# Kernel tuning notes

Hardware: AMD Instinct MI355X
Metric: run time of the kernel (lower is better)

Reference implementation:

```python
import jax, jax.numpy as jnp
import numpy as np

N = 50000      # nodes
E = 800000     # edges
INS = 128
H = 128
OUTS = 128
G = 512        # graphs in batch
BN_EPS = 1e-5


def _lin(k, fan_in, fan_out):
    s = 1.0 / np.sqrt(fan_in)
    kw, kb = jax.random.split(k)
    w = jax.random.uniform(kw, (fan_in, fan_out), minval=-s, maxval=s, dtype=jnp.float32)
    b = jax.random.uniform(kb, (fan_out,), minval=-s, maxval=s, dtype=jnp.float32)
    return w, b


def setup_inputs() -> dict:
    key = jax.random.key(0)
    ks = jax.random.split(key, 16)
    x = jax.random.normal(ks[0], (N, INS), dtype=jnp.float32)
    edge_src = jax.random.randint(ks[1], (E,), 0, N, dtype=jnp.int32)
    edge_dst = jax.random.randint(ks[2], (E,), 0, N, dtype=jnp.int32)
    ptr = jnp.sort(jax.random.randint(ks[3], (G + 1,), 0, N, dtype=jnp.int32))
    ptr = ptr.at[0].set(0).at[-1].set(N)
    w1a, b1a = _lin(ks[4], INS, H)
    w1b, b1b = _lin(ks[5], H, H)
    w2a, b2a = _lin(ks[6], H, H)
    w2b, b2b = _lin(ks[7], H, H)
    w3a, b3a = _lin(ks[8], H, H)
    w3b, b3b = _lin(ks[9], H, OUTS)
    g1 = jnp.ones((H,), jnp.float32); be1 = jnp.zeros((H,), jnp.float32)
    g2 = jnp.ones((H,), jnp.float32); be2 = jnp.zeros((H,), jnp.float32)
    g3 = jnp.ones((H,), jnp.float32); be3 = jnp.zeros((H,), jnp.float32)
    return dict(x=x, edge_src=edge_src, edge_dst=edge_dst, ptr=ptr,
                w1a=w1a, b1a=b1a, g1=g1, be1=be1, w1b=w1b, b1b=b1b,
                w2a=w2a, b2a=b2a, g2=g2, be2=be2, w2b=w2b, b2b=b2b,
                w3a=w3a, b3a=b3a, g3=g3, be3=be3, w3b=w3b, b3b=b3b)


def _bn(h, gamma, beta):
    # BatchNorm1d in training mode: stats over the node dimension
    mu = jnp.mean(h, axis=0)
    var = jnp.var(h, axis=0)
    return gamma * (h - mu) * jax.lax.rsqrt(var + BN_EPS) + beta


def _gin_layer(h, src, dst, wa, ba, gamma, beta, wb, bb):
    # GINConv (eps=0): mlp(x + sum_{j in N(i)} x_j)
    agg = jax.ops.segment_sum(h[src], dst, num_segments=N)  # [N, d]
    h = h + agg
    h = jax.nn.relu(_bn(h @ wa + ba, gamma, beta))
    h = jax.nn.relu(h @ wb + bb)
    return h


def reference(x, edge_src, edge_dst, ptr,
              w1a, b1a, g1, be1, w1b, b1b,
              w2a, b2a, g2, be2, w2b, b2b,
              w3a, b3a, g3, be3, w3b, b3b):
    h = _gin_layer(x, edge_src, edge_dst, w1a, b1a, g1, be1, w1b, b1b)
    h = _gin_layer(h, edge_src, edge_dst, w2a, b2a, g2, be2, w2b, b2b)
    h = _gin_layer(h, edge_src, edge_dst, w3a, b3a, g3, be3, w3b, b3b)
    # segment_csr(x, ptr, reduce='sum') readout
    seg = jnp.searchsorted(ptr, jnp.arange(N, dtype=jnp.int32), side='right') - 1
    return jax.ops.segment_sum(h, seg, num_segments=G)  # [G, OUTS]
```

## Files before the change

### kernel.cpp

```cpp
#include <hip/hip_runtime.h>

#define NNODES 50000
#define NEDGES 800000
#define HD 128
#define NG 512
#define BN_EPS 1e-5f
#define NTILE 3125
#define NSPLIT 8
#define NSB 49
#define AROW 136

typedef short bf16x8 __attribute__((ext_vector_type(8)));
typedef float floatx4 __attribute__((ext_vector_type(4)));

union U16 { uint4 u; bf16x8 h; };

__device__ __forceinline__ ushort f2bf(float f) {
    unsigned u = __float_as_uint(f);
    return (ushort)((u + 0x7fffu + ((u >> 16) & 1u)) >> 16);
}
__device__ __forceinline__ void unpack8(const uint4& u, float* f) {
    const unsigned* w = (const unsigned*)&u;
#pragma unroll
    for (int i = 0; i < 4; ++i) {
        f[2 * i]     = __uint_as_float(w[i] << 16);
        f[2 * i + 1] = __uint_as_float(w[i] & 0xffff0000u);
    }
}
__device__ __forceinline__ uint4 pack8(const float* f) {
    uint4 o;
    unsigned* w = (unsigned*)&o;
#pragma unroll
    for (int i = 0; i < 4; ++i)
        w[i] = (unsigned)f2bf(f[2 * i]) | ((unsigned)f2bf(f[2 * i + 1]) << 16);
    return o;
}


struct WP6 { const float* w[6]; };

__global__ __launch_bounds__(256) void prep_kernel(
    const int* __restrict__ edst, int* __restrict__ cnt, int* __restrict__ rank,
    WP6 p, ushort* __restrict__ wf) {
    const int b = blockIdx.x, t = threadIdx.x;
    if (b < 3125) {
        int i = b * 256 + t;
        rank[i] = atomicAdd(&cnt[edst[i]], 1);
    } else {
        int m = b - 3125;
        const float* W = p.w[m];
        ushort* o = wf + (size_t)m * 16384;
        for (int i = t; i < 16384; i += 256) {
            int j = i & 7, lane = (i >> 3) & 63, kc = (i >> 9) & 3, ct = i >> 11;
            int k = kc * 32 + (lane >> 4) * 8 + j;
            int n = ct * 16 + (lane & 15);
            o[i] = f2bf(W[k * HD + n]);
        }
    }
}


__global__ void scan1_kernel(const int* __restrict__ cnt, int* __restrict__ incl,
                             int* __restrict__ bsum, int n) {
    __shared__ int s[1024];
    int i = blockIdx.x * 1024 + threadIdx.x;
    int v = (i < n) ? cnt[i] : 0;
    s[threadIdx.x] = v;
    __syncthreads();
    for (int off = 1; off < 1024; off <<= 1) {
        int add = (threadIdx.x >= off) ? s[threadIdx.x - off] : 0;
        __syncthreads();
        s[threadIdx.x] += add;
        __syncthreads();
    }
    if (i < n) incl[i] = s[threadIdx.x];
    if (threadIdx.x == 1023) bsum[blockIdx.x] = s[1023];
}

__global__ void scan23_kernel(const int* __restrict__ incl, const int* __restrict__ bsum,
                              int* __restrict__ rowp, int n) {
    __shared__ int bpre[64];
    const int t = threadIdx.x;
    if (t < 64) {
        int own = (t < NSB) ? bsum[t] : 0;
        int v = own;
        for (int off = 1; off < 64; off <<= 1) {
            int u = __shfl_up(v, off);
            if (t >= off) v += u;
        }
        bpre[t] = v - own;
    }
    __syncthreads();
    int i = blockIdx.x * 256 + t;
    if (i < n) rowp[i + 1] = incl[i] + bpre[i >> 10];
    if (i == 0) rowp[0] = 0;
}

__global__ void build_kernel(const int* __restrict__ src, const int* __restrict__ dst,
                             const int* __restrict__ rowp, const int* __restrict__ rank,
                             int* __restrict__ colv, int n) {
    int i = blockIdx.x * 256 + threadIdx.x;
    if (i < n) colv[rowp[dst[i]] + rank[i]] = src[i];
}


__global__ __launch_bounds__(256, 4) void gemm0A_kernel(
    const float* __restrict__ x, const ushort* __restrict__ Wf,
    ushort* __restrict__ y) {
    __shared__ ushort abuf[16 * AROW];
    __shared__ ushort cbuf[16 * HD];
    const int t = threadIdx.x;
    const int wave = t >> 6, lane = t & 63;
    const int quad = lane >> 4, l16 = lane & 15;
    const int row0 = blockIdx.x * 16;

    const uint4* Wf4 = (const uint4*)Wf;
    uint4 bfr[2][4];
#pragma unroll
    for (int c = 0; c < 2; ++c)
#pragma unroll
        for (int kc = 0; kc < 4; ++kc)
            bfr[c][kc] = Wf4[((2 * wave + c) * 4 + kc) * 64 + lane];

    {
        int r = t >> 4, l = t & 15;
        const float* xp = x + (size_t)(row0 + r) * HD + l * 8;
        float4 v0 = ((const float4*)xp)[0];
        float4 v1 = ((const float4*)xp)[1];
        float f[8] = {v0.x, v0.y, v0.z, v0.w, v1.x, v1.y, v1.z, v1.w};
        *(uint4*)&abuf[r * AROW + l * 8] = pack8(f);
    }
    __syncthreads();

    U16 afr[4];
#pragma unroll
    for (int kc = 0; kc < 4; ++kc)
        afr[kc].u = *(const uint4*)&abuf[l16 * AROW + kc * 32 + quad * 8];

    floatx4 zf = {0.f, 0.f, 0.f, 0.f};
    floatx4 acc[2] = {zf, zf};
#pragma unroll
    for (int kc = 0; kc < 4; ++kc)
#pragma unroll
        for (int c = 0; c < 2; ++c) {
            U16 bu; bu.u = bfr[c][kc];
            acc[c] = __builtin_amdgcn_mfma_f32_16x16x32_bf16(afr[kc].h, bu.h, acc[c], 0, 0, 0);
        }

    const int lrow = quad * 4;
#pragma unroll
    for (int c = 0; c < 2; ++c) {
        int col = (2 * wave + c) * 16 + l16;
#pragma unroll
        for (int reg = 0; reg < 4; ++reg)
            cbuf[(lrow + reg) * HD + col] = f2bf(acc[c][reg]);
    }
    __syncthreads();
    {
        const uint4* c4 = (const uint4*)cbuf;
        uint4* o4 = (uint4*)y;
        int row = t >> 4, part = t & 15;
        o4[(size_t)(row0 + row) * 16 + part] = c4[t];
    }
}


__global__ __launch_bounds__(256) void agg_kernel(
    const ushort* __restrict__ y, const int* __restrict__ rowp,
    const int* __restrict__ colv, const float* __restrict__ bias,
    ushort* __restrict__ z, float* __restrict__ ssum_p, float* __restrict__ ssq_p) {
    __shared__ float reds[4][HD];
    __shared__ float redq[4][HD];
    const int t = threadIdx.x;
    const int wave = t >> 6, lane = t & 63;
    const int node = blockIdx.x * 16 + (t >> 4);
    const int l = t & 15;
    const uint4* hp = (const uint4*)y;

    float a[8];
    unpack8(hp[(size_t)node * 16 + l], a);
    int beg = rowp[node], end = rowp[node + 1];
    for (int j = beg; j < end; ++j) {
        float b[8];
        unpack8(hp[(size_t)colv[j] * 16 + l], b);
#pragma unroll
        for (int i = 0; i < 8; ++i) a[i] += b[i];
    }
    {
        float4 b0 = ((const float4*)(bias + l * 8))[0];
        float4 b1 = ((const float4*)(bias + l * 8))[1];
        a[0] += b0.x; a[1] += b0.y; a[2] += b0.z; a[3] += b0.w;
        a[4] += b1.x; a[5] += b1.y; a[6] += b1.z; a[7] += b1.w;
    }
    ((uint4*)z)[(size_t)node * 16 + l] = pack8(a);

    float s[8], q[8];
#pragma unroll
    for (int i = 0; i < 8; ++i) { s[i] = a[i]; q[i] = a[i] * a[i]; }
#pragma unroll
    for (int i = 0; i < 8; ++i) {
        s[i] += __shfl_xor(s[i], 16); s[i] += __shfl_xor(s[i], 32);
        q[i] += __shfl_xor(q[i], 16); q[i] += __shfl_xor(q[i], 32);
    }
    if (lane < 16) {
#pragma unroll
        for (int i = 0; i < 8; ++i) {
            reds[wave][lane * 8 + i] = s[i];
            redq[wave][lane * 8 + i] = q[i];
        }
    }
    __syncthreads();
    int slot = (blockIdx.x & (NSPLIT - 1)) * HD;
    if (t < HD) {
        atomicAdd(&ssum_p[slot + t], reds[0][t] + reds[1][t] + reds[2][t] + reds[3][t]);
    } else if (t < 2 * HD) {
        int c = t - HD;
        atomicAdd(&ssq_p[slot + c], redq[0][c] + redq[1][c] + redq[2][c] + redq[3][c]);
    }
}


__global__ __launch_bounds__(256, 3) void gemmBA_kernel(
    const ushort* __restrict__ z, const ushort* __restrict__ WfB,
    const ushort* __restrict__ WfA2, const float* __restrict__ biasB,
    ushort* __restrict__ yout,
    const float* __restrict__ gamma, const float* __restrict__ beta,
    const float* __restrict__ ssum_p, const float* __restrict__ ssq_p) {
    __shared__ ushort was[16384];
    __shared__ ushort cbuf[16 * AROW];
    __shared__ float sca[HD];
    __shared__ float shf[HD];
    const int t = threadIdx.x;
    const int wave = t >> 6, lane = t & 63;
    const int quad = lane >> 4, l16 = lane & 15;
    const int row0 = blockIdx.x * 16;
    const int rowA = row0 + l16;

    {
        const uint4* g = (const uint4*)WfA2;
        uint4 v[8];
#pragma unroll
        for (int i = 0; i < 8; ++i) v[i] = g[i * 256 + t];
        uint4* s = (uint4*)was;
#pragma unroll
        for (int i = 0; i < 8; ++i) s[i * 256 + t] = v[i];
    }

    const uint4* Wf4 = (const uint4*)WfB;
    uint4 bfr[2][4];
#pragma unroll
    for (int c = 0; c < 2; ++c)
#pragma unroll
        for (int kc = 0; kc < 4; ++kc)
            bfr[c][kc] = Wf4[((2 * wave + c) * 4 + kc) * 64 + lane];

    U16 afr[4];
    {
        const ushort* ap = z + (size_t)rowA * HD + quad * 8;
#pragma unroll
        for (int kc = 0; kc < 4; ++kc)
            afr[kc].u = *(const uint4*)(ap + kc * 32);
    }

    if (t < HD) {
        float s = 0.f, q = 0.f;
#pragma unroll
        for (int i = 0; i < NSPLIT; ++i) { s += ssum_p[i * HD + t]; q += ssq_p[i * HD + t]; }
        float mean = s / (float)NNODES;
        float var = q / (float)NNODES - mean * mean;
        float rstd = rsqrtf(var + BN_EPS);
        float sc = gamma[t] * rstd;
        sca[t] = sc;
        shf[t] = beta[t] - mean * sc;
    }
    __syncthreads();

#pragma unroll
    for (int kc = 0; kc < 4; ++kc) {
        float f[8];
        unpack8(afr[kc].u, f);
        int kb = kc * 32 + quad * 8;
        float4 s0 = ((const float4*)(sca + kb))[0];
        float4 s1 = ((const float4*)(sca + kb))[1];
        float4 h0 = ((const float4*)(shf + kb))[0];
        float4 h1 = ((const float4*)(shf + kb))[1];
        f[0] = fmaxf(fmaf(f[0], s0.x, h0.x), 0.f);
        f[1] = fmaxf(fmaf(f[1], s0.y, h0.y), 0.f);
        f[2] = fmaxf(fmaf(f[2], s0.z, h0.z), 0.f);
        f[3] = fmaxf(fmaf(f[3], s0.w, h0.w), 0.f);
        f[4] = fmaxf(fmaf(f[4], s1.x, h1.x), 0.f);
        f[5] = fmaxf(fmaf(f[5], s1.y, h1.y), 0.f);
        f[6] = fmaxf(fmaf(f[6], s1.z, h1.z), 0.f);
        f[7] = fmaxf(fmaf(f[7], s1.w, h1.w), 0.f);
        afr[kc].u = pack8(f);
    }

    floatx4 zf = {0.f, 0.f, 0.f, 0.f};
    floatx4 acc[2] = {zf, zf};
#pragma unroll
    for (int kc = 0; kc < 4; ++kc)
#pragma unroll
        for (int c = 0; c < 2; ++c) {
            U16 bu; bu.u = bfr[c][kc];
            acc[c] = __builtin_amdgcn_mfma_f32_16x16x32_bf16(afr[kc].h, bu.h, acc[c], 0, 0, 0);
        }

    const int lrow = quad * 4;
#pragma unroll
    for (int c = 0; c < 2; ++c) {
        int col = (2 * wave + c) * 16 + l16;
        float b = biasB[col];
#pragma unroll
        for (int reg = 0; reg < 4; ++reg)
            cbuf[(lrow + reg) * AROW + col] = f2bf(fmaxf(acc[c][reg] + b, 0.f));
    }
    __syncthreads();

    U16 a2[4];
#pragma unroll
    for (int kc = 0; kc < 4; ++kc)
        a2[kc].u = *(const uint4*)&cbuf[l16 * AROW + kc * 32 + quad * 8];
    const uint4* W2 = (const uint4*)was;
    floatx4 acc2[2] = {zf, zf};
#pragma unroll
    for (int kc = 0; kc < 4; ++kc)
#pragma unroll
        for (int c = 0; c < 2; ++c) {
            U16 bu; bu.u = W2[((2 * wave + c) * 4 + kc) * 64 + lane];
            acc2[c] = __builtin_amdgcn_mfma_f32_16x16x32_bf16(a2[kc].h, bu.h, acc2[c], 0, 0, 0);
        }
    __syncthreads();

#pragma unroll
    for (int c = 0; c < 2; ++c) {
        int col = (2 * wave + c) * 16 + l16;
#pragma unroll
        for (int reg = 0; reg < 4; ++reg)
            cbuf[(lrow + reg) * AROW + col] = f2bf(acc2[c][reg]);
    }
    __syncthreads();
    {
        uint4* o4 = (uint4*)yout;
        int row = t >> 4, part = t & 15;
        o4[(size_t)(row0 + row) * 16 + part] = *(const uint4*)&cbuf[row * AROW + part * 8];
    }
}


__global__ __launch_bounds__(256, 4) void gemmB2_kernel(
    const ushort* __restrict__ z, const ushort* __restrict__ WfB,
    const float* __restrict__ biasB,
    const float* __restrict__ gamma, const float* __restrict__ beta,
    const float* __restrict__ ssum_p, const float* __restrict__ ssq_p,
    const int* __restrict__ gptr, float* __restrict__ gout) {
    __shared__ float sca[HD];
    __shared__ float shf[HD];
    const int t = threadIdx.x;
    const int wave = t >> 6, lane = t & 63;
    const int quad = lane >> 4, l16 = lane & 15;
    const int row0 = blockIdx.x * 16;
    const int rowA = row0 + l16;

    const uint4* Wf4 = (const uint4*)WfB;
    uint4 bfr[2][4];
#pragma unroll
    for (int c = 0; c < 2; ++c)
#pragma unroll
        for (int kc = 0; kc < 4; ++kc)
            bfr[c][kc] = Wf4[((2 * wave + c) * 4 + kc) * 64 + lane];

    U16 afr[4];
    {
        const ushort* ap = z + (size_t)rowA * HD + quad * 8;
#pragma unroll
        for (int kc = 0; kc < 4; ++kc)
            afr[kc].u = *(const uint4*)(ap + kc * 32);
    }

    if (t < HD) {
        float s = 0.f, q = 0.f;
#pragma unroll
        for (int i = 0; i < NSPLIT; ++i) { s += ssum_p[i * HD + t]; q += ssq_p[i * HD + t]; }
        float mean = s / (float)NNODES;
        float var = q / (float)NNODES - mean * mean;
        float rstd = rsqrtf(var + BN_EPS);
        float sc = gamma[t] * rstd;
        sca[t] = sc;
        shf[t] = beta[t] - mean * sc;
    }
    __syncthreads();

#pragma unroll
    for (int kc = 0; kc < 4; ++kc) {
        float f[8];
        unpack8(afr[kc].u, f);
        int kb = kc * 32 + quad * 8;
        float4 s0 = ((const float4*)(sca + kb))[0];
        float4 s1 = ((const float4*)(sca + kb))[1];
        float4 h0 = ((const float4*)(shf + kb))[0];
        float4 h1 = ((const float4*)(shf + kb))[1];
        f[0] = fmaxf(fmaf(f[0], s0.x, h0.x), 0.f);
        f[1] = fmaxf(fmaf(f[1], s0.y, h0.y), 0.f);
        f[2] = fmaxf(fmaf(f[2], s0.z, h0.z), 0.f);
        f[3] = fmaxf(fmaf(f[3], s0.w, h0.w), 0.f);
        f[4] = fmaxf(fmaf(f[4], s1.x, h1.x), 0.f);
        f[5] = fmaxf(fmaf(f[5], s1.y, h1.y), 0.f);
        f[6] = fmaxf(fmaf(f[6], s1.z, h1.z), 0.f);
        f[7] = fmaxf(fmaf(f[7], s1.w, h1.w), 0.f);
        afr[kc].u = pack8(f);
    }

    floatx4 zf = {0.f, 0.f, 0.f, 0.f};
    floatx4 acc[2] = {zf, zf};
#pragma unroll
    for (int kc = 0; kc < 4; ++kc)
#pragma unroll
        for (int c = 0; c < 2; ++c) {
            U16 bu; bu.u = bfr[c][kc];
            acc[c] = __builtin_amdgcn_mfma_f32_16x16x32_bf16(afr[kc].h, bu.h, acc[c], 0, 0, 0);
        }

    int r_base = row0 + quad * 4;
    int lo = 0, hi = NG - 1;
    while (lo < hi) {
        int mid = (lo + hi) >> 1;
        if (r_base >= gptr[mid + 1]) lo = mid + 1; else hi = mid;
    }
    int segr[4];
    int sg = lo;
#pragma unroll
    for (int reg = 0; reg < 4; ++reg) {
        while (r_base + reg >= gptr[sg + 1]) ++sg;
        segr[reg] = sg;
    }
#pragma unroll
    for (int c = 0; c < 2; ++c) {
        int col = (2 * wave + c) * 16 + l16;
        float b = biasB[col];
        float run = 0.f;
        int cur = segr[0];
#pragma unroll
        for (int reg = 0; reg < 4; ++reg) {
            if (segr[reg] != cur) {
                if (run != 0.f) atomicAdd(&gout[cur * HD + col], run);
                run = 0.f;
                cur = segr[reg];
            }
            run += fmaxf(acc[c][reg] + b, 0.f);
        }
        if (run != 0.f) atomicAdd(&gout[cur * HD + col], run);
    }
}


extern "C" void kernel_launch(void* const* d_in, const int* in_sizes, int n_in,
                              void* d_out, int out_size, void* d_ws, size_t ws_size,
                              hipStream_t stream) {
    const float* x = (const float*)d_in[0];
    const int* esrc = (const int*)d_in[1];
    const int* edst = (const int*)d_in[2];
    const int* gptr = (const int*)d_in[3];
    const float* wA[3] = {(const float*)d_in[4], (const float*)d_in[10], (const float*)d_in[16]};
    const float* bA[3] = {(const float*)d_in[5], (const float*)d_in[11], (const float*)d_in[17]};
    const float* gm[3] = {(const float*)d_in[6], (const float*)d_in[12], (const float*)d_in[18]};
    const float* bt[3] = {(const float*)d_in[7], (const float*)d_in[13], (const float*)d_in[19]};
    const float* wB[3] = {(const float*)d_in[8], (const float*)d_in[14], (const float*)d_in[20]};
    const float* bB[3] = {(const float*)d_in[9], (const float*)d_in[15], (const float*)d_in[21]};

    char* w = (char*)d_ws;
    ushort* ybuf = (ushort*)w; w += (size_t)NNODES * HD * 2;
    ushort* zbuf = (ushort*)w; w += (size_t)NNODES * HD * 2;
    ushort* wf   = (ushort*)w; w += (size_t)6 * 16384 * 2;
    int* colv  = (int*)w;   w += (size_t)NEDGES * 4;
    int* rank  = (int*)w;   w += (size_t)NEDGES * 4;
    int* incl  = (int*)w;   w += (size_t)NNODES * 4;
    int* rowp  = (int*)w;   w += ((size_t)(NNODES + 1) * 4 + 15) & ~(size_t)15;
    int* bsum  = (int*)w;   w += 64 * 4;
    char* zero_base = w;
    int* cnt   = (int*)w;   w += (size_t)NNODES * 4;
    float* ssum_p = (float*)w; w += 3 * NSPLIT * 128 * 4;
    float* ssq_p  = (float*)w; w += 3 * NSPLIT * 128 * 4;
    size_t zero_bytes = (size_t)(w - zero_base);

    hipMemsetAsync(zero_base, 0, zero_bytes, stream);
    hipMemsetAsync(d_out, 0, (size_t)NG * HD * 4, stream);

    WP6 wp;
    wp.w[0] = wA[0]; wp.w[1] = wB[0]; wp.w[2] = wA[1];
    wp.w[3] = wB[1]; wp.w[4] = wA[2]; wp.w[5] = wB[2];

    prep_kernel<<<3131, 256, 0, stream>>>(edst, cnt, rank, wp, wf);
    scan1_kernel<<<NSB, 1024, 0, stream>>>(cnt, incl, bsum, NNODES);
    scan23_kernel<<<(NNODES + 255) / 256, 256, 0, stream>>>(incl, bsum, rowp, NNODES);
    build_kernel<<<(NEDGES + 255) / 256, 256, 0, stream>>>(esrc, edst, rowp, rank, colv, NEDGES);

    gemm0A_kernel<<<NTILE, 256, 0, stream>>>(x, wf, ybuf);

    for (int l = 0; l < 3; ++l) {
        agg_kernel<<<NTILE, 256, 0, stream>>>(
            ybuf, rowp, colv, bA[l], zbuf,
            ssum_p + l * NSPLIT * 128, ssq_p + l * NSPLIT * 128);
        if (l < 2) {
            gemmBA_kernel<<<NTILE, 256, 0, stream>>>(
                zbuf, wf + (size_t)(2 * l + 1) * 16384, wf + (size_t)(2 * l + 2) * 16384,
                bB[l], ybuf, gm[l], bt[l],
                ssum_p + l * NSPLIT * 128, ssq_p + l * NSPLIT * 128);
        } else {
            gemmB2_kernel<<<NTILE, 256, 0, stream>>>(
                zbuf, wf + (size_t)(2 * l + 1) * 16384, bB[l], gm[l], bt[l],
                ssum_p + l * NSPLIT * 128, ssq_p + l * NSPLIT * 128,
                gptr, (float*)d_out);
        }
    }
}
```

Measured before the change: 402.9 us.

## Fuse first GEMM into prep kernel, single-pass scan, unroll edge gather

Merges the first-layer GEMM into the prep kernel, where each GEMM block converts W1a into a shared-memory bf16 tile itself. Replaces the two-kernel scan with a single chained scan that passes block prefixes through flags in global memory. Unrolls the aggregation gather by four so more neighbour loads are in flight at once. These changes cut two kernel launches and expose more memory-level parallelism. The cost is a redundant per-block weight conversion, a 32KB+ LDS footprint that lowers occupancy, and a serial dependency between scan blocks.

```diff
diff --git a/kernel.cpp b/kernel.cpp
--- a/kernel.cpp
+++ b/kernel.cpp
@@ -39,15 +39,22 @@
 
 struct WP6 { const float* w[6]; };
 
-__global__ __launch_bounds__(256) void prep_kernel(
+__global__ __launch_bounds__(256, 3) void prep_kernel(
     const int* __restrict__ edst, int* __restrict__ cnt, int* __restrict__ rank,
-    WP6 p, ushort* __restrict__ wf) {
+    WP6 p, ushort* __restrict__ wf,
+    const float* __restrict__ x, ushort* __restrict__ y) {
+    __shared__ ushort wls[16384];
+    __shared__ ushort abuf[16 * AROW];
+    __shared__ ushort cbuf[16 * HD];
     const int b = blockIdx.x, t = threadIdx.x;
+
     if (b < 3125) {
         int i = b * 256 + t;
         rank[i] = atomicAdd(&cnt[edst[i]], 1);
-    } else {
-        int m = b - 3125;
+        return;
+    }
+    if (b < 3130) {
+        int m = b - 3125 + 1;
         const float* W = p.w[m];
         ushort* o = wf + (size_t)m * 16384;
         for (int i = t; i < 16384; i += 256) {
@@ -56,71 +63,31 @@
             int n = ct * 16 + (lane & 15);
             o[i] = f2bf(W[k * HD + n]);
         }
-    }
-}
-
-
-__global__ void scan1_kernel(const int* __restrict__ cnt, int* __restrict__ incl,
-                             int* __restrict__ bsum, int n) {
-    __shared__ int s[1024];
-    int i = blockIdx.x * 1024 + threadIdx.x;
-    int v = (i < n) ? cnt[i] : 0;
-    s[threadIdx.x] = v;
-    __syncthreads();
-    for (int off = 1; off < 1024; off <<= 1) {
-        int add = (threadIdx.x >= off) ? s[threadIdx.x - off] : 0;
-        __syncthreads();
-        s[threadIdx.x] += add;
-        __syncthreads();
-    }
-    if (i < n) incl[i] = s[threadIdx.x];
-    if (threadIdx.x == 1023) bsum[blockIdx.x] = s[1023];
-}
-
-__global__ void scan23_kernel(const int* __restrict__ incl, const int* __restrict__ bsum,
-                              int* __restrict__ rowp, int n) {
-    __shared__ int bpre[64];
-    const int t = threadIdx.x;
-    if (t < 64) {
-        int own = (t < NSB) ? bsum[t] : 0;
-        int v = own;
-        for (int off = 1; off < 64; off <<= 1) {
-            int u = __shfl_up(v, off);
-            if (t >= off) v += u;
-        }
-        bpre[t] = v - own;
-    }
-    __syncthreads();
-    int i = blockIdx.x * 256 + t;
-    if (i < n) rowp[i + 1] = incl[i] + bpre[i >> 10];
-    if (i == 0) rowp[0] = 0;
-}
-
-__global__ void build_kernel(const int* __restrict__ src, const int* __restrict__ dst,
-                             const int* __restrict__ rowp, const int* __restrict__ rank,
-                             int* __restrict__ colv, int n) {
-    int i = blockIdx.x * 256 + threadIdx.x;
-    if (i < n) colv[rowp[dst[i]] + rank[i]] = src[i];
-}
-
-
-__global__ __launch_bounds__(256, 4) void gemm0A_kernel(
-    const float* __restrict__ x, const ushort* __restrict__ Wf,
-    ushort* __restrict__ y) {
-    __shared__ ushort abuf[16 * AROW];
-    __shared__ ushort cbuf[16 * HD];
-    const int t = threadIdx.x;
+        return;
+    }
+
+    const int row0 = (b - 3130) * 16;
     const int wave = t >> 6, lane = t & 63;
     const int quad = lane >> 4, l16 = lane & 15;
-    const int row0 = blockIdx.x * 16;
-
-    const uint4* Wf4 = (const uint4*)Wf;
-    uint4 bfr[2][4];
-#pragma unroll
-    for (int c = 0; c < 2; ++c)
-#pragma unroll
-        for (int kc = 0; kc < 4; ++kc)
-            bfr[c][kc] = Wf4[((2 * wave + c) * 4 + kc) * 64 + lane];
+
+    {
+        const float* W = p.w[0];
+        int k = t >> 1;
+        int n0 = (t & 1) * 64;
+        int kc = k >> 5, quad_w = (k >> 3) & 3, j = k & 7;
+        int base = quad_w * 16 * 8 + j;
+#pragma unroll
+        for (int e = 0; e < 64; e += 4) {
+            float4 v = *(const float4*)(W + (size_t)k * HD + n0 + e);
+            float f[4] = {v.x, v.y, v.z, v.w};
+#pragma unroll
+            for (int q = 0; q < 4; ++q) {
+                int n = n0 + e + q;
+                int ct = n >> 4, lw = n & 15;
+                wls[((ct * 4 + kc) * 64) * 8 + base + lw * 8] = f2bf(f[q]);
+            }
+        }
+    }
 
     {
         int r = t >> 4, l = t & 15;
@@ -137,13 +104,14 @@
     for (int kc = 0; kc < 4; ++kc)
         afr[kc].u = *(const uint4*)&abuf[l16 * AROW + kc * 32 + quad * 8];
 
+    const uint4* B4 = (const uint4*)wls;
     floatx4 zf = {0.f, 0.f, 0.f, 0.f};
     floatx4 acc[2] = {zf, zf};
 #pragma unroll
     for (int kc = 0; kc < 4; ++kc)
 #pragma unroll
         for (int c = 0; c < 2; ++c) {
-            U16 bu; bu.u = bfr[c][kc];
+            U16 bu; bu.u = B4[((2 * wave + c) * 4 + kc) * 64 + lane];
             acc[c] = __builtin_amdgcn_mfma_f32_16x16x32_bf16(afr[kc].h, bu.h, acc[c], 0, 0, 0);
         }
 
@@ -162,6 +130,46 @@
         int row = t >> 4, part = t & 15;
         o4[(size_t)(row0 + row) * 16 + part] = c4[t];
     }
+}
+
+
+__global__ __launch_bounds__(1024) void scan_kernel(
+    const int* __restrict__ cnt, int* __restrict__ bflag,
+    int* __restrict__ rowp, int n) {
+    __shared__ int s[1024];
+    __shared__ int sprefix;
+    const int t = threadIdx.x;
+    const int bid = blockIdx.x;
+    int i = bid * 1024 + t;
+    int v = (i < n) ? cnt[i] : 0;
+    s[t] = v;
+    __syncthreads();
+    for (int off = 1; off < 1024; off <<= 1) {
+        int add = (t >= off) ? s[t - off] : 0;
+        __syncthreads();
+        s[t] += add;
+        __syncthreads();
+    }
+    if (t == 0) {
+        int pre = 0;
+        if (bid > 0) {
+            int f;
+            do { f = atomicAdd(&bflag[bid - 1], 0); } while (f == 0);
+            pre = f - 1;
+        }
+        atomicExch(&bflag[bid], pre + s[1023] + 1);
+        sprefix = pre;
+    }
+    __syncthreads();
+    if (i < n) rowp[i + 1] = s[t] + sprefix;
+    if (i == 0) rowp[0] = 0;
+}
+
+__global__ void build_kernel(const int* __restrict__ src, const int* __restrict__ dst,
+                             const int* __restrict__ rowp, const int* __restrict__ rank,
+                             int* __restrict__ colv, int n) {
+    int i = blockIdx.x * 256 + threadIdx.x;
+    if (i < n) colv[rowp[dst[i]] + rank[i]] = src[i];
 }
 
 
@@ -180,7 +188,19 @@
     float a[8];
     unpack8(hp[(size_t)node * 16 + l], a);
     int beg = rowp[node], end = rowp[node + 1];
-    for (int j = beg; j < end; ++j) {
+    int j = beg;
+    for (; j + 3 < end; j += 4) {
+        int c0 = colv[j], c1 = colv[j + 1], c2 = colv[j + 2], c3 = colv[j + 3];
+        uint4 v0 = hp[(size_t)c0 * 16 + l];
+        uint4 v1 = hp[(size_t)c1 * 16 + l];
+        uint4 v2 = hp[(size_t)c2 * 16 + l];
+        uint4 v3 = hp[(size_t)c3 * 16 + l];
+        float b0[8], b1[8], b2[8], b3[8];
+        unpack8(v0, b0); unpack8(v1, b1); unpack8(v2, b2); unpack8(v3, b3);
+#pragma unroll
+        for (int i = 0; i < 8; ++i) a[i] += (b0[i] + b1[i]) + (b2[i] + b3[i]);
+    }
+    for (; j < end; ++j) {
         float b[8];
         unpack8(hp[(size_t)colv[j] * 16 + l], b);
 #pragma unroll
@@ -473,11 +493,10 @@
     ushort* wf   = (ushort*)w; w += (size_t)6 * 16384 * 2;
     int* colv  = (int*)w;   w += (size_t)NEDGES * 4;
     int* rank  = (int*)w;   w += (size_t)NEDGES * 4;
-    int* incl  = (int*)w;   w += (size_t)NNODES * 4;
     int* rowp  = (int*)w;   w += ((size_t)(NNODES + 1) * 4 + 15) & ~(size_t)15;
-    int* bsum  = (int*)w;   w += 64 * 4;
     char* zero_base = w;
     int* cnt   = (int*)w;   w += (size_t)NNODES * 4;
+    int* bflag = (int*)w;   w += 64 * 4;
     float* ssum_p = (float*)w; w += 3 * NSPLIT * 128 * 4;
     float* ssq_p  = (float*)w; w += 3 * NSPLIT * 128 * 4;
     size_t zero_bytes = (size_t)(w - zero_base);
@@ -489,12 +508,9 @@
     wp.w[0] = wA[0]; wp.w[1] = wB[0]; wp.w[2] = wA[1];
     wp.w[3] = wB[1]; wp.w[4] = wA[2]; wp.w[5] = wB[2];
 
-    prep_kernel<<<3131, 256, 0, stream>>>(edst, cnt, rank, wp, wf);
-    scan1_kernel<<<NSB, 1024, 0, stream>>>(cnt, incl, bsum, NNODES);
-    scan23_kernel<<<(NNODES + 255) / 256, 256, 0, stream>>>(incl, bsum, rowp, NNODES);
+    prep_kernel<<<6255, 256, 0, stream>>>(edst, cnt, rank, wp, wf, x, ybuf);
+    scan_kernel<<<NSB, 1024, 0, stream>>>(cnt, bflag, rowp, NNODES);
     build_kernel<<<(NEDGES + 255) / 256, 256, 0, stream>>>(esrc, edst, rowp, rank, colv, NEDGES);
-
-    gemm0A_kernel<<<NTILE, 256, 0, stream>>>(x, wf, ybuf);
 
     for (int l = 0; l < 3; ++l) {
         agg_kernel<<<NTILE, 256, 0, stream>>>(
```

Result: slower. 415.7 us (+3.2%).
